# Performance work log

Measured on AMD Instinct MI355X. Metric: run time of the kernel, lower is better.

The kernel has to match this reference:

```python
import jax, jax.numpy as jnp
from jax import lax
import numpy as np

B, P, D = 32, 196, 2048   # batch, num_pixels (14x14), encoder_dim
A, E, H, V = 512, 512, 512, 10000  # attention_dim, embed_dim, decoder_dim, vocab
L = 21                    # max caption length -> T = 20 decode steps


def setup_inputs() -> dict:
    key = jax.random.key(0)
    ks = jax.random.split(key, 16)
    def n(k, shape, s=0.02):
        return jax.random.normal(k, shape, jnp.float32) * s
    def u(k, shape):
        return jax.random.uniform(k, shape, jnp.float32, -0.1, 0.1)
    caption_lengths = jnp.concatenate(
        [jnp.array([[L]], dtype=jnp.int32),
         jax.random.randint(ks[1], (B - 1, 1), 8, L + 1)], axis=0)
    return dict(
        encoder_out=jax.random.normal(ks[0], (B, P, D), jnp.float32) * 0.5,
        encoded_captions=jax.random.randint(ks[2], (B, L), 0, V),
        caption_lengths=caption_lengths,
        enc_att_w=n(ks[3], (D, A)), enc_att_b=jnp.zeros((A,), jnp.float32),
        dec_att_w=n(ks[4], (H, A)), dec_att_b=jnp.zeros((A,), jnp.float32),
        full_att_w=n(ks[5], (A,)), full_att_b=jnp.zeros((), jnp.float32),
        emb=u(ks[6], (V, E)),
        init_h_w=n(ks[7], (D, H)), init_h_b=jnp.zeros((H,), jnp.float32),
        init_c_w=n(ks[8], (D, H)), init_c_b=jnp.zeros((H,), jnp.float32),
        f_beta_w=n(ks[9], (H, D)), f_beta_b=jnp.zeros((D,), jnp.float32),
        lstm_w_ih=n(ks[10], (E + D, 4 * H)),
        lstm_w_hh=n(ks[11], (H, 4 * H)),
        lstm_b=jnp.zeros((4 * H,), jnp.float32),
        fc_w=u(ks[12], (H, V)), fc_b=jnp.zeros((V,), jnp.float32),
    )


def reference(encoder_out, encoded_captions, caption_lengths,
              enc_att_w, enc_att_b, dec_att_w, dec_att_b, full_att_w, full_att_b,
              emb, init_h_w, init_h_b, init_c_w, init_c_b,
              f_beta_w, f_beta_b, lstm_w_ih, lstm_w_hh, lstm_b, fc_w, fc_b):
    # sort batch by caption length, descending (matches torch .sort descending=True)
    lengths = caption_lengths[:, 0]
    sort_ind = jnp.argsort(-lengths)
    lengths = lengths[sort_ind]
    enc = encoder_out[sort_ind]                 # [B,P,D]
    caps = encoded_captions[sort_ind]           # [B,L]
    embs = emb[caps]                            # [B,L,E]

    mean_enc = enc.mean(axis=1)                 # [B,D]
    h0 = mean_enc @ init_h_w + init_h_b         # [B,H]
    c0 = mean_enc @ init_c_w + init_c_b

    # encoder branch of additive attention is constant across timesteps
    att1 = enc @ enc_att_w + enc_att_b          # [B,P,A]
    dec_lens = lengths - 1                      # [B]
    T = caps.shape[1] - 1

    def step(carry, xs):
        h, c = carry
        emb_t, t = xs                            # [B,E], scalar
        att2 = h @ dec_att_w + dec_att_b         # [B,A]
        e = jnp.einsum('bpa,a->bp', jax.nn.relu(att1 + att2[:, None, :]), full_att_w) + full_att_b
        alpha = jax.nn.softmax(e, axis=1)        # [B,P]
        awe = jnp.einsum('bpd,bp->bd', enc, alpha)
        gate = jax.nn.sigmoid(h @ f_beta_w + f_beta_b)
        awe = gate * awe                         # [B,D]
        x = jnp.concatenate([emb_t, awe], axis=-1)  # [B,E+D]
        g = x @ lstm_w_ih + h @ lstm_w_hh + lstm_b  # [B,4H] gates i,f,g,o
        i_g, f_g, g_g, o_g = jnp.split(g, 4, axis=-1)
        c_new = jax.nn.sigmoid(f_g) * c + jax.nn.sigmoid(i_g) * jnp.tanh(g_g)
        h_new = jax.nn.sigmoid(o_g) * jnp.tanh(c_new)
        preds = h_new @ fc_w + fc_b              # [B,V] (dropout = identity, eval mode)
        active = (t < dec_lens)[:, None]         # length-based batch slicing -> mask
        h = jnp.where(active, h_new, h)
        c = jnp.where(active, c_new, c)
        preds = jnp.where(active, preds, 0.0)
        alpha = jnp.where(active, alpha, 0.0)
        return (h, c), (preds, alpha)

    xs = (jnp.swapaxes(embs[:, :T], 0, 1), jnp.arange(T))
    (_, _), (preds, alphas) = lax.scan(step, (h0, c0), xs)
    predictions = jnp.swapaxes(preds, 0, 1)      # [B,T,V]
    alphas = jnp.swapaxes(alphas, 0, 1)          # [B,T,P]
    return predictions, caps, dec_lens, alphas, sort_ind
```

## Files before the change

kernel.cpp:

```cpp
#include <hip/hip_runtime.h>

#define B_ 32
#define P_ 196
#define D_ 2048
#define A_ 512
#define E_ 512
#define H_ 512
#define V_ 10000
#define L_ 21
#define T_ 20
#define PP 208

typedef unsigned short us;

struct KParams {
  const float* encoder_out; const int* captions; const int* cap_lens;
  const float* enc_att_w; const float* enc_att_b;
  const float* dec_att_w; const float* dec_att_b;
  const float* full_att_w; const float* full_att_b;
  const float* emb;
  const float* init_h_w; const float* init_h_b;
  const float* init_c_w; const float* init_c_b;
  const float* f_beta_w; const float* f_beta_b;
  const float* lstm_w_ih; const float* lstm_w_hh; const float* lstm_b;
  const float* fc_w; const float* fc_b;
  float* out_preds; float* out_caps; float* out_declens; float* out_alphas; float* out_sortind;
  int* sort_ind; int* declen; int* caps_s;
  us* h_bf16; float* c; us* mean_bf16;
  us* waw_bf16; us* wihE_bf16; us* embs_bf16;
  us* att1; us* Wt; us* Wt2; us* Wt3; us* encT; us* awe_bf16;
  float* gpre; float* s1out; float* alpha_g;
  int* sync;
};

__device__ __forceinline__ us f2bf(float x){
  unsigned u = __float_as_uint(x);
  unsigned r = ((u >> 16) & 1u) + 0x7FFFu;
  return (us)((u + r) >> 16);
}
__device__ __forceinline__ unsigned pack2(float a, float b){
  return (unsigned)f2bf(a) | ((unsigned)f2bf(b) << 16);
}
__device__ __forceinline__ float bf2f(unsigned u16){ return __uint_as_float(u16 << 16); }
__device__ __forceinline__ float sigm(float x){ return 1.f/(1.f + __expf(-x)); }
__device__ __forceinline__ float tanh_f(float x){ return 1.f - 2.f/(__expf(2.f*x) + 1.f); }

__device__ __forceinline__ unsigned ald(const unsigned* p){
  return __hip_atomic_load(p, __ATOMIC_RELAXED, __HIP_MEMORY_SCOPE_AGENT);
}
__device__ __forceinline__ void ast(unsigned* p, unsigned v){
  __hip_atomic_store(p, v, __ATOMIC_RELAXED, __HIP_MEMORY_SCOPE_AGENT);
}
__device__ __forceinline__ float aldf(const float* p){
  return __uint_as_float(ald((const unsigned*)p));
}
__device__ __forceinline__ void astf(float* p, float v){
  ast((unsigned*)p, __float_as_uint(v));
}

using bf16x8 = __attribute__((ext_vector_type(8))) short;
using f32x4  = __attribute__((ext_vector_type(4))) float;
#define MFMA(a,b,c) __builtin_amdgcn_mfma_f32_16x16x32_bf16((a),(b),(c),0,0,0)

#define HS 528
#define AS 2064


__global__ void k_meta(KParams p){
  __shared__ int len[32], sidx[32], sdecl[32];
  int tid = threadIdx.x;
  if (tid < 32) len[tid] = p.cap_lens[tid];
  __syncthreads();
  if (tid == 0){
    bool used[32];
    for (int i = 0; i < 32; i++) used[i] = false;
    for (int r = 0; r < 32; r++){
      int best = -1, bl = -2;
      for (int i = 0; i < 32; i++) if (!used[i] && len[i] > bl){ bl = len[i]; best = i; }
      used[best] = true; sidx[r] = best; sdecl[r] = bl - 1;
    }
  }
  __syncthreads();
  if (tid < 32){
    p.sort_ind[tid] = sidx[tid]; p.out_sortind[tid] = (float)sidx[tid];
    p.declen[tid]   = sdecl[tid]; p.out_declens[tid] = (float)sdecl[tid];
  }
  for (int idx = tid; idx < B_*L_; idx += 64){
    int b = idx / L_, l = idx - b*L_;
    int cv = p.captions[sidx[b]*L_ + l];
    p.caps_s[idx] = cv; p.out_caps[idx] = (float)cv;
  }
}

__device__ void tp64(const float* src, us* dst, int R, int C, int Rp, int bi){
  __shared__ float tl[64][68];
  int tilesC = (C + 63) >> 6;
  int tr = bi / tilesC, tc = bi - tr*tilesC;
  int r0 = tr << 6, c0 = tc << 6;
  int tid = threadIdx.x;
  {
    int r = tid >> 2, cs = (tid & 3) << 4;
    bool rok = (r0 + r) < R;
    #pragma unroll
    for (int i = 0; i < 4; i++){
      int c = c0 + cs + i*4;
      float4 v = make_float4(0.f, 0.f, 0.f, 0.f);
      if (rok && c < C) v = *(const float4*)(src + (size_t)(r0 + r)*C + c);
      *(float4*)&tl[r][cs + i*4] = v;
    }
  }
  __syncthreads();
  {
    int c = tid >> 2, rs = (tid & 3) << 4;
    if (c0 + c < C && r0 + rs < Rp){
      us tmp[16];
      #pragma unroll
      for (int i = 0; i < 16; i++) tmp[i] = f2bf(tl[rs + i][c]);
      *(uint4*)(dst + (size_t)(c0 + c)*Rp + r0 + rs)     = *(uint4*)&tmp[0];
      *(uint4*)(dst + (size_t)(c0 + c)*Rp + r0 + rs + 8) = *(uint4*)&tmp[8];
    }
  }
}

__global__ void k_prep(KParams p){
  int bi = blockIdx.x, tid = threadIdx.x;
  if (bi < 512){
    #pragma unroll
    for (int i = 0; i < 4; i++){
      int q = bi*1024 + i*256 + tid;
      const float4* src; uint2* dst; int qq;
      if (q < 262144){ src = (const float4*)p.enc_att_w; dst = (uint2*)p.waw_bf16;  qq = q; }
      else           { src = (const float4*)p.lstm_w_ih; dst = (uint2*)p.wihE_bf16; qq = q - 262144; }
      float4 v = src[qq];
      dst[qq] = make_uint2(pack2(v.x, v.y), pack2(v.z, v.w));
    }
  } else if (bi < 576){   tp64(p.dec_att_w, p.Wt,             512, 512,   512,  bi - 512);
  } else if (bi < 832){   tp64(p.f_beta_w,  p.Wt + 512*512,   512, 2048,  512,  bi - 576);
  } else if (bi < 1088){  tp64(p.lstm_w_hh, p.Wt + 2560*512,  512, 2048,  512,  bi - 832);
  } else if (bi < 2344){  tp64(p.fc_w,      p.Wt + 4608*512,  512, 10000, 512,  bi - 1088);
  } else if (bi < 3368){  tp64(p.lstm_w_ih + 512*2048, p.Wt2, 2048, 2048, 2048, bi - 2344);
  } else if (bi < 3624){  tp64(p.init_h_w,  p.Wt3,            2048, 512,  2048, bi - 3368);
  } else if (bi < 3880){  tp64(p.init_c_w,  p.Wt3 + 512*2048, 2048, 512,  2048, bi - 3624);
  } else if (bi < 4200){
    int q = (bi - 3880)*256 + tid;
    int row = q >> 7, qi = q & 127;
    int t = row >> 5, b = row & 31;
    int cap = p.caps_s[b*L_ + t];
    float4 v = ((const float4*)(p.emb + (size_t)cap*E_))[qi];
    ((uint2*)p.embs_bf16)[q] = make_uint2(pack2(v.x, v.y), pack2(v.z, v.w));
  } else {
    int bl = bi - 4200;
    int b = bl >> 7, ti = bl & 127;
    tp64(p.encoder_out + (size_t)p.sort_ind[b]*(P_*D_), p.encT + (size_t)b*D_*PP,
         196, 2048, PP, ti);
  }
}

__global__ void __launch_bounds__(256) k_gemm2(KParams p){
  __shared__ us a_lds[128][40];
  __shared__ us b_lds[128][40];
  int bi = blockIdx.x;
  const us* Aq = nullptr; const float* Af = nullptr; const int* sidx = nullptr;
  const us* Bq; const float* bias; float* C; int N, K, obf, mode, ti;
  if (bi < 196){
    Af = p.encoder_out; sidx = p.sort_ind; Bq = p.waw_bf16; bias = p.enc_att_b;
    C = (float*)p.att1; N = 512; K = 2048; obf = 1; mode = 1; ti = bi;
  } else {
    Aq = p.embs_bf16; Bq = p.wihE_bf16; bias = p.lstm_b;
    C = p.gpre; N = 2048; K = 512; obf = 0; mode = 0; ti = bi - 196;
  }
  int ntiles = N >> 7;
  int bm = (ti / ntiles) << 7;
  int bn = (ti % ntiles) << 7;
  int tid = threadIdx.x;
  int wave = tid >> 6, lane = tid & 63;
  int wr = (wave >> 1) << 6, wc = (wave & 1) << 6;
  int la = lane & 15, lq = lane >> 4;
  f32x4 acc[4][4] = {};
  for (int k0 = 0; k0 < K; k0 += 32){
    {
      int r = tid >> 1, ch = (tid & 1) << 4;
      if (mode == 0){
        const uint4* asrc = (const uint4*)(Aq + (size_t)(bm + r)*K + k0 + ch);
        uint4 v0 = asrc[0], v1 = asrc[1];
        *(uint4*)&a_lds[r][ch]     = v0;
        *(uint4*)&a_lds[r][ch + 8] = v1;
      } else {
        int g = bm + r; int b = g / 196; int pp = g - b*196;
        const float4* as = (const float4*)(Af + ((size_t)sidx[b]*196 + pp)*2048 + k0 + ch);
        float4 f0 = as[0], f1 = as[1], f2 = as[2], f3 = as[3];
        *(uint4*)&a_lds[r][ch]     = make_uint4(pack2(f0.x,f0.y), pack2(f0.z,f0.w), pack2(f1.x,f1.y), pack2(f1.z,f1.w));
        *(uint4*)&a_lds[r][ch + 8] = make_uint4(pack2(f2.x,f2.y), pack2(f2.z,f2.w), pack2(f3.x,f3.y), pack2(f3.z,f3.w));
      }
      int kk = tid >> 3, n0 = (tid & 7) << 4;
      const us* bs = Bq + (size_t)(k0 + kk)*N + bn + n0;
      uint4 bv0 = *(const uint4*)bs, bv1 = *(const uint4*)(bs + 8);
      unsigned vals[8] = {bv0.x, bv0.y, bv0.z, bv0.w, bv1.x, bv1.y, bv1.z, bv1.w};
      #pragma unroll
      for (int i = 0; i < 8; i++){
        b_lds[n0 + 2*i][kk]     = (us)(vals[i] & 0xffffu);
        b_lds[n0 + 2*i + 1][kk] = (us)(vals[i] >> 16);
      }
    }
    __syncthreads();
    bf16x8 af[4], bfr[4];
    #pragma unroll
    for (int mt = 0; mt < 4; mt++) af[mt]  = *(const bf16x8*)&a_lds[wr + mt*16 + la][lq*8];
    #pragma unroll
    for (int nt = 0; nt < 4; nt++) bfr[nt] = *(const bf16x8*)&b_lds[wc + nt*16 + la][lq*8];
    #pragma unroll
    for (int mt = 0; mt < 4; mt++)
      #pragma unroll
      for (int nt = 0; nt < 4; nt++)
        acc[mt][nt] = MFMA(af[mt], bfr[nt], acc[mt][nt]);
    __syncthreads();
  }
  #pragma unroll
  for (int mt = 0; mt < 4; mt++){
    int row0 = bm + wr + mt*16 + lq*4;
    #pragma unroll
    for (int nt = 0; nt < 4; nt++){
      int coln = bn + wc + nt*16 + la;
      float bb = bias ? bias[coln] : 0.f;
      #pragma unroll
      for (int r = 0; r < 4; r++){
        float v = acc[mt][nt][r] + bb;
        if (obf) ((us*)C)[(size_t)(row0 + r)*N + coln] = f2bf(v);
        else     C[(size_t)(row0 + r)*N + coln] = v;
      }
    }
  }
}


__device__ __forceinline__ void gsync_g(int* sc, int gen, int jb){
  __syncthreads();
  if (threadIdx.x == 0){
    int old = __hip_atomic_fetch_add(&sc[(jb & 7)*32], 1, __ATOMIC_RELEASE, __HIP_MEMORY_SCOPE_AGENT);
    bool last = false;
    if (old == gen*4 - 1){
      int old2 = __hip_atomic_fetch_add(&sc[512], 1, __ATOMIC_RELAXED, __HIP_MEMORY_SCOPE_AGENT);
      if (old2 == gen*8 - 1){
        __hip_atomic_store(&sc[544], gen, __ATOMIC_RELEASE, __HIP_MEMORY_SCOPE_AGENT);
        last = true;
      }
    }
    if (!last){
      while (__hip_atomic_load(&sc[544], __ATOMIC_RELAXED, __HIP_MEMORY_SCOPE_AGENT) < gen)
        __builtin_amdgcn_s_sleep(2);
    }
  }
  __syncthreads();
}

__device__ __forceinline__ void fc_run(const KParams& p, const int* sm_dl, const us* hlds,
                                       int b0, int slot, int nslots, int niter,
                                       int la, int lq, int tpred){
  bf16x8 afr[16];
  #pragma unroll
  for (int ks = 0; ks < 16; ks++) afr[ks] = *(const bf16x8*)&hlds[(la & 3)*HS + lq*8 + ks*32];
  for (int it = 0; it < niter; it++){
    int tile = slot + it*nslots;
    if (tile < 625){
      int n0 = tile*16;
      const us* wp = p.Wt + ((size_t)(4608 + n0 + la))*512 + lq*8;
      f32x4 ac = {};
      #pragma unroll
      for (int ks = 0; ks < 16; ks++){
        bf16x8 bB = *(const bf16x8*)(wp + ks*32);
        ac = MFMA(afr[ks], bB, ac);
      }
      if (lq == 0){
        int v = n0 + la;
        float bb = p.fc_b[v];
        #pragma unroll
        for (int r = 0; r < 4; r++){
          bool act = tpred < sm_dl[b0 + r];
          p.out_preds[((size_t)(b0 + r)*T_ + tpred)*V_ + v] = act ? (ac[r] + bb) : 0.f;
        }
      }
    }
  }
}

__global__ void __launch_bounds__(512, 2) k_loop(KParams p){
  const int tid = threadIdx.x, blk = blockIdx.x;
  const int gb = blk >> 5, jb = blk & 31, b0 = gb*4;
  const int wv = tid >> 6, lane = tid & 63, la = lane & 15, lq = lane >> 4;
  int* sc = p.sync + gb*1024;
  __shared__ float sm_att2[512], sm_fw[512], sm_red[16];
  __shared__ float sm_a4f[4*PP];
  __shared__ float gq2[4][2][16][4];
  __shared__ int sm_dl[32];
  __shared__ us sm_h[4*HS];
  __shared__ us sm_awe[4*AS];
  int gen = 0;

  if (tid < 32) sm_dl[tid] = p.declen[tid];
  __syncthreads();

  {
    int part = tid & 1, pair = tid >> 1;
    int d = jb*64 + (pair >> 2), b = b0 + (pair & 3);
    const uint4* rp = (const uint4*)(p.encT + ((size_t)b*D_ + d)*PP);
    int cs = part*13;
    float s = 0.f;
    for (int i = cs; i < cs + 13; i++){
      uint4 u = rp[i];
      s += bf2f(u.x&0xffffu)+bf2f(u.x>>16)+bf2f(u.y&0xffffu)+bf2f(u.y>>16)
         + bf2f(u.z&0xffffu)+bf2f(u.z>>16)+bf2f(u.w&0xffffu)+bf2f(u.w>>16);
    }
    s += __shfl_xor(s, 1);
    float mv = s*(1.f/196.f);
    float ov = __shfl_xor(mv, 8);
    if (part == 0 && !(tid & 8))
      ast((unsigned*)p.mean_bf16 + ((size_t)b*1024 + (d >> 1)), pack2(mv, ov));
  }
  gsync_g(sc, ++gen, jb);
  if (jb < 8){
    {
      unsigned* dst = (unsigned*)sm_awe;
      const unsigned* src = (const unsigned*)p.mean_bf16 + (size_t)b0*1024;
      for (int i = tid; i < 4096; i += 512) dst[(i >> 10)*(AS >> 1) + (i & 1023)] = ald(src + i);
    }
    __syncthreads();
    int slot = jb*8 + wv;
    const us* wp = p.Wt3 + ((size_t)(slot*16 + la))*2048 + lq*8;
    const us* ap = sm_awe + (la & 3)*AS + lq*8;
    f32x4 ac0 = {}, ac1 = {};
    for (int ki = 0; ki < 64; ki += 2){
      bf16x8 aA = *(const bf16x8*)(ap + ki*32);
      bf16x8 bB = *(const bf16x8*)(wp + ki*32);
      ac0 = MFMA(aA, bB, ac0);
      bf16x8 aA2 = *(const bf16x8*)(ap + ki*32 + 32);
      bf16x8 bB2 = *(const bf16x8*)(wp + ki*32 + 32);
      ac1 = MFMA(aA2, bB2, ac1);
    }
    f32x4 ac = ac0 + ac1;
    int col = slot*16 + la;
    if (col < 512){
      #pragma unroll
      for (int r = 0; r < 4; r++){
        float v0 = ac[r] + p.init_h_b[col];
        float v1 = __shfl_xor(v0, 1);
        if (lq == 0 && !(la & 1))
          ast((unsigned*)p.h_bf16 + (((size_t)(b0+r)*512 + col) >> 1), pack2(v0, v1));
      }
    } else {
      #pragma unroll
      for (int r = 0; r < 4; r++)
        if (lq == 0) astf(&p.c[(size_t)(b0+r)*512 + col - 512], ac[r] + p.init_c_b[col - 512]);
    }
  }
  gsync_g(sc, ++gen, jb);

  for (int t = 0; t < T_; ++t){
    {
      unsigned* dst = (unsigned*)sm_h;
      const unsigned* src = (const unsigned*)p.h_bf16 + (size_t)b0*256;
      for (int i = tid; i < 1024; i += 512) dst[(i >> 8)*(HS >> 1) + (i & 255)] = ald(src + i);
    }
    __syncthreads();
    {
      int slot = jb*8 + wv;
      bf16x8 afr[16];
      #pragma unroll
      for (int ks = 0; ks < 16; ks++) afr[ks] = *(const bf16x8*)&sm_h[(la & 3)*HS + lq*8 + ks*32];
      int tiles2[2];
      tiles2[0] = slot;
      tiles2[1] = (slot < 32) ? (256 + slot) : -1;
      #pragma unroll
      for (int it = 0; it < 2; it++){
        int tile = tiles2[it];
        if (tile >= 0){
          int n0 = tile*16;
          const us* wp = p.Wt + ((size_t)(n0 + la))*512 + lq*8;
          f32x4 ac = {};
          #pragma unroll
          for (int ks = 0; ks < 16; ks++){
            bf16x8 bB = *(const bf16x8*)(wp + ks*32);
            ac = MFMA(afr[ks], bB, ac);
          }
          if (lq == 0){
            #pragma unroll
            for (int r = 0; r < 4; r++) astf(&p.s1out[(size_t)(b0+r)*4608 + n0 + la], ac[r]);
          }
        }
      }
    }
    gsync_g(sc, ++gen, jb);
    if (jb < 4){
      int b = b0 + jb;
      for (int cc = tid; cc < 512; cc += 512){
        sm_att2[cc] = aldf(&p.s1out[(size_t)b*4608 + cc]) + p.dec_att_b[cc];
        sm_fw[cc]   = p.full_att_w[cc];
      }
      __syncthreads();
      float ee = -1e30f;
      if (tid < 196){
        const uint4* row = (const uint4*)(p.att1 + ((size_t)(b*196 + tid))*512);
        float s = 0.f;
        #pragma unroll 8
        for (int i = 0; i < 64; i++){
          uint4 u = row[i];
          float4 a0 = *(const float4*)&sm_att2[i*8], a1 = *(const float4*)&sm_att2[i*8+4];
          float4 f0 = *(const float4*)&sm_fw[i*8],   f1 = *(const float4*)&sm_fw[i*8+4];
          s += fmaxf(bf2f(u.x&0xffffu)+a0.x,0.f)*f0.x + fmaxf(bf2f(u.x>>16)+a0.y,0.f)*f0.y
             + fmaxf(bf2f(u.y&0xffffu)+a0.z,0.f)*f0.z + fmaxf(bf2f(u.y>>16)+a0.w,0.f)*f0.w
             + fmaxf(bf2f(u.z&0xffffu)+a1.x,0.f)*f1.x + fmaxf(bf2f(u.z>>16)+a1.y,0.f)*f1.y
             + fmaxf(bf2f(u.w&0xffffu)+a1.z,0.f)*f1.z + fmaxf(bf2f(u.w>>16)+a1.w,0.f)*f1.w;
        }
        ee = s;
      }
      float v = ee;
      #pragma unroll
      for (int off = 32; off; off >>= 1) v = fmaxf(v, __shfl_xor(v, off));
      if (lane == 0) sm_red[wv] = v;
      __syncthreads();
      float m = sm_red[0];
      #pragma unroll
      for (int i = 1; i < 8; i++) m = fmaxf(m, sm_red[i]);
      float ex = (tid < 196) ? __expf(ee - m) : 0.f;
      float sv = ex;
      #pragma unroll
      for (int off = 32; off; off >>= 1) sv += __shfl_xor(sv, off);
      if (lane == 0) sm_red[8 + wv] = sv;
      __syncthreads();
      float ssum = sm_red[8];
      #pragma unroll
      for (int i = 1; i < 8; i++) ssum += sm_red[8 + i];
      if (tid < 196){
        float a = ex/ssum;
        astf(&p.alpha_g[b*PP + tid], a);
        bool act = t < sm_dl[b];
        p.out_alphas[((size_t)b*T_ + t)*P_ + tid] = act ? a : 0.f;
      } else if (tid < PP) astf(&p.alpha_g[b*PP + tid], 0.f);
    } else if (t > 0){
      fc_run(p, sm_dl, sm_h, b0, (jb - 4)*8 + wv, 224, 3, la, lq, t - 1);
    }
    gsync_g(sc, ++gen, jb);
    {
      for (int i = tid; i < 4*PP; i += 512) sm_a4f[i] = aldf(&p.alpha_g[b0*PP + i]);
      __syncthreads();
      int part = tid & 1, pair = tid >> 1;
      int d = jb*64 + (pair >> 2), b = b0 + (pair & 3);
      const float* al = sm_a4f + (pair & 3)*PP;
      const uint4* rp = (const uint4*)(p.encT + ((size_t)b*D_ + d)*PP);
      int cs = part*13;
      float acc = 0.f;
      for (int i = cs; i < cs + 13; i++){
        uint4 u = rp[i];
        float4 a0 = *(const float4*)(al + i*8), a1 = *(const float4*)(al + i*8 + 4);
        acc += a0.x*bf2f(u.x&0xffffu) + a0.y*bf2f(u.x>>16)
             + a0.z*bf2f(u.y&0xffffu) + a0.w*bf2f(u.y>>16)
             + a1.x*bf2f(u.z&0xffffu) + a1.y*bf2f(u.z>>16)
             + a1.z*bf2f(u.w&0xffffu) + a1.w*bf2f(u.w>>16);
      }
      acc += __shfl_xor(acc, 1);
      float gate = sigm(aldf(&p.s1out[(size_t)b*4608 + 512 + d]) + p.f_beta_b[d]);
      float wv_ = acc*gate;
      float ov = __shfl_xor(wv_, 8);
      if (part == 0 && !(tid & 8))
        ast((unsigned*)p.awe_bf16 + ((size_t)b*1024 + (d >> 1)), pack2(wv_, ov));
    }
    gsync_g(sc, ++gen, jb);
    {
      {
        unsigned* dst = (unsigned*)sm_awe;
        const unsigned* src = (const unsigned*)p.awe_bf16 + (size_t)b0*1024;
        for (int i = tid; i < 4096; i += 512) dst[(i >> 10)*(AS >> 1) + (i & 1023)] = ald(src + i);
      }
      __syncthreads();
      int q = wv >> 1, kh = wv & 1, hc0 = jb*16;
      const us* wp = p.Wt2 + ((size_t)(q*512 + hc0 + la))*2048 + kh*1024 + lq*8;
      const us* ap = sm_awe + (la & 3)*AS + kh*1024 + lq*8;
      f32x4 ac0 = {}, ac1 = {};
      for (int ki = 0; ki < 32; ki += 2){
        bf16x8 aA = *(const bf16x8*)(ap + ki*32);
        bf16x8 bB = *(const bf16x8*)(wp + ki*32);
        ac0 = MFMA(aA, bB, ac0);
        bf16x8 aA2 = *(const bf16x8*)(ap + ki*32 + 32);
        bf16x8 bB2 = *(const bf16x8*)(wp + ki*32 + 32);
        ac1 = MFMA(aA2, bB2, ac1);
      }
      f32x4 ac = ac0 + ac1;
      if (lq == 0){
        #pragma unroll
        for (int r = 0; r < 4; r++) gq2[q][kh][la][r] = ac[r];
      }
      __syncthreads();
      if (tid < 64){
        int hc = hc0 + (tid & 15), r = tid >> 4;
        int b = b0 + r;
        float gv[4];
        #pragma unroll
        for (int qq = 0; qq < 4; qq++)
          gv[qq] = gq2[qq][0][tid & 15][r] + gq2[qq][1][tid & 15][r]
                 + aldf(&p.s1out[(size_t)b*4608 + 2560 + qq*512 + hc])
                 + p.gpre[((size_t)t*32 + b)*2048 + qq*512 + hc];
        float cold = aldf(&p.c[(size_t)b*512 + hc]);
        float cn = sigm(gv[1])*cold + sigm(gv[0])*tanh_f(gv[2]);
        float hn = sigm(gv[3])*tanh_f(cn);
        float hv1 = __shfl_xor(hn, 1);
        if (t < sm_dl[b]){
          astf(&p.c[(size_t)b*512 + hc], cn);
          if (!(tid & 1))
            ast((unsigned*)p.h_bf16 + (((size_t)b*512 + hc) >> 1), pack2(hn, hv1));
        }
      }
    }
    gsync_g(sc, ++gen, jb);
  }
  {
    unsigned* dst = (unsigned*)sm_h;
    const unsigned* src = (const unsigned*)p.h_bf16 + (size_t)b0*256;
    for (int i = tid; i < 1024; i += 512) dst[(i >> 8)*(HS >> 1) + (i & 255)] = ald(src + i);
  }
  __syncthreads();
  fc_run(p, sm_dl, sm_h, b0, jb*8 + wv, 256, 3, la, lq, T_ - 1);
}


extern "C" void kernel_launch(void* const* d_in, const int* in_sizes, int n_in,
                              void* d_out, int out_size, void* d_ws, size_t ws_size,
                              hipStream_t stream){
  (void)in_sizes; (void)n_in; (void)out_size; (void)ws_size;
  KParams p;
  p.encoder_out = (const float*)d_in[0];
  p.captions    = (const int*)d_in[1];
  p.cap_lens    = (const int*)d_in[2];
  p.enc_att_w   = (const float*)d_in[3];  p.enc_att_b = (const float*)d_in[4];
  p.dec_att_w   = (const float*)d_in[5];  p.dec_att_b = (const float*)d_in[6];
  p.full_att_w  = (const float*)d_in[7];  p.full_att_b = (const float*)d_in[8];
  p.emb         = (const float*)d_in[9];
  p.init_h_w    = (const float*)d_in[10]; p.init_h_b = (const float*)d_in[11];
  p.init_c_w    = (const float*)d_in[12]; p.init_c_b = (const float*)d_in[13];
  p.f_beta_w    = (const float*)d_in[14]; p.f_beta_b = (const float*)d_in[15];
  p.lstm_w_ih   = (const float*)d_in[16]; p.lstm_w_hh = (const float*)d_in[17]; p.lstm_b = (const float*)d_in[18];
  p.fc_w        = (const float*)d_in[19]; p.fc_b = (const float*)d_in[20];

  float* out = (float*)d_out;
  p.out_preds   = out;
  p.out_caps    = out + 6400000;
  p.out_declens = out + 6400672;
  p.out_alphas  = out + 6400704;
  p.out_sortind = out + 6526144;

  char* w = (char*)d_ws; size_t off = 0;
  auto alloc = [&](size_t bytes)->char*{ char* r = w + off; off = (off + bytes + 255) & ~(size_t)255; return r; };
  p.sort_ind  = (int*)alloc(128);
  p.declen    = (int*)alloc(128);
  p.caps_s    = (int*)alloc(2688);
  p.h_bf16    = (us*)alloc(32768);
  p.c         = (float*)alloc(65536);
  p.mean_bf16 = (us*)alloc(131072);
  p.waw_bf16  = (us*)alloc(2097152);
  p.wihE_bf16 = (us*)alloc(2097152);
  p.embs_bf16 = (us*)alloc(655360);
  p.att1      = (us*)alloc(6422528);
  p.Wt        = (us*)alloc(14958592);
  p.Wt2       = (us*)alloc(8388608);
  p.Wt3       = (us*)alloc(4194304);
  p.encT      = (us*)alloc(27262976);
  p.gpre      = (float*)alloc(5242880);
  p.s1out     = (float*)alloc(589824);
  p.alpha_g   = (float*)alloc(26624);
  p.awe_bf16  = (us*)alloc(131072);
  p.sync      = (int*)alloc(32768);

  hipMemsetAsync(p.sync, 0, 32768, stream);
  hipLaunchKernelGGL(k_meta,  dim3(1),    dim3(64),  0, stream, p);
  hipLaunchKernelGGL(k_prep,  dim3(8296), dim3(256), 0, stream, p);
  hipLaunchKernelGGL(k_gemm2, dim3(276),  dim3(256), 0, stream, p);
  void* args[] = { (void*)&p };
  hipLaunchCooperativeKernel((void*)k_loop, dim3(256), dim3(512), args, 0, stream);
}
```

Baseline: 1.571 ms.

## Fuse h-projection stage into attention/FC stage and simplify grid barrier

Removes one grid-wide barrier per decode step. The attention blocks now compute their own dec_att projection of h redundantly into shared memory. The remaining blocks compute the f_beta and w_hh projections of h together with the previous step's FC output tiles in one distributed loop. The hierarchical atomic barrier is also replaced by a single-counter spin barrier with no sleep. This cuts sync latency, but costs redundant MFMA work in the four attention blocks and more contention on the single atomic counter.

Measured after the change: 1.660 ms. 5.7% more time.

```diff
diff --git a/kernel.cpp b/kernel.cpp
--- a/kernel.cpp
+++ b/kernel.cpp
@@ -233,22 +233,11 @@
 }
 
 
-__device__ __forceinline__ void gsync_g(int* sc, int gen, int jb){
+__device__ __forceinline__ void gsync_g(int* sc, int gen){
   __syncthreads();
   if (threadIdx.x == 0){
-    int old = __hip_atomic_fetch_add(&sc[(jb & 7)*32], 1, __ATOMIC_RELEASE, __HIP_MEMORY_SCOPE_AGENT);
-    bool last = false;
-    if (old == gen*4 - 1){
-      int old2 = __hip_atomic_fetch_add(&sc[512], 1, __ATOMIC_RELAXED, __HIP_MEMORY_SCOPE_AGENT);
-      if (old2 == gen*8 - 1){
-        __hip_atomic_store(&sc[544], gen, __ATOMIC_RELEASE, __HIP_MEMORY_SCOPE_AGENT);
-        last = true;
-      }
-    }
-    if (!last){
-      while (__hip_atomic_load(&sc[544], __ATOMIC_RELAXED, __HIP_MEMORY_SCOPE_AGENT) < gen)
-        __builtin_amdgcn_s_sleep(2);
-    }
+    __hip_atomic_fetch_add(&sc[0], 1, __ATOMIC_RELEASE, __HIP_MEMORY_SCOPE_AGENT);
+    while (__hip_atomic_load(&sc[0], __ATOMIC_RELAXED, __HIP_MEMORY_SCOPE_AGENT) < gen*32) {}
   }
   __syncthreads();
 }
@@ -316,7 +305,7 @@
     if (part == 0 && !(tid & 8))
       ast((unsigned*)p.mean_bf16 + ((size_t)b*1024 + (d >> 1)), pack2(mv, ov));
   }
-  gsync_g(sc, ++gen, jb);
+  gsync_g(sc, ++gen);
   if (jb < 8){
     {
       unsigned* dst = (unsigned*)sm_awe;
@@ -352,7 +341,7 @@
         if (lq == 0) astf(&p.c[(size_t)(b0+r)*512 + col - 512], ac[r] + p.init_c_b[col - 512]);
     }
   }
-  gsync_g(sc, ++gen, jb);
+  gsync_g(sc, ++gen);
 
   for (int t = 0; t < T_; ++t){
     {
@@ -361,39 +350,23 @@
       for (int i = tid; i < 1024; i += 512) dst[(i >> 8)*(HS >> 1) + (i & 255)] = ald(src + i);
     }
     __syncthreads();
-    {
-      int slot = jb*8 + wv;
-      bf16x8 afr[16];
-      #pragma unroll
-      for (int ks = 0; ks < 16; ks++) afr[ks] = *(const bf16x8*)&sm_h[(la & 3)*HS + lq*8 + ks*32];
-      int tiles2[2];
-      tiles2[0] = slot;
-      tiles2[1] = (slot < 32) ? (256 + slot) : -1;
-      #pragma unroll
-      for (int it = 0; it < 2; it++){
-        int tile = tiles2[it];
-        if (tile >= 0){
-          int n0 = tile*16;
-          const us* wp = p.Wt + ((size_t)(n0 + la))*512 + lq*8;
-          f32x4 ac = {};
-          #pragma unroll
-          for (int ks = 0; ks < 16; ks++){
-            bf16x8 bB = *(const bf16x8*)(wp + ks*32);
-            ac = MFMA(afr[ks], bB, ac);
-          }
-          if (lq == 0){
-            #pragma unroll
-            for (int r = 0; r < 4; r++) astf(&p.s1out[(size_t)(b0+r)*4608 + n0 + la], ac[r]);
-          }
-        }
-      }
-    }
-    gsync_g(sc, ++gen, jb);
+    bf16x8 afr[16];
+    #pragma unroll
+    for (int ks = 0; ks < 16; ks++) afr[ks] = *(const bf16x8*)&sm_h[(la & 3)*HS + lq*8 + ks*32];
     if (jb < 4){
       int b = b0 + jb;
-      for (int cc = tid; cc < 512; cc += 512){
-        sm_att2[cc] = aldf(&p.s1out[(size_t)b*4608 + cc]) + p.dec_att_b[cc];
-        sm_fw[cc]   = p.full_att_w[cc];
+      for (int cc = tid; cc < 512; cc += 512) sm_fw[cc] = p.full_att_w[cc];
+      #pragma unroll
+      for (int tt = 0; tt < 4; tt++){
+        int n0 = (wv*4 + tt)*16;
+        const us* wp = p.Wt + ((size_t)(n0 + la))*512 + lq*8;
+        f32x4 ac = {};
+        #pragma unroll
+        for (int ks = 0; ks < 16; ks++){
+          bf16x8 bB = *(const bf16x8*)(wp + ks*32);
+          ac = MFMA(afr[ks], bB, ac);
+        }
+        if (lq == 0) sm_att2[n0 + la] = ac[jb] + p.dec_att_b[n0 + la];
       }
       __syncthreads();
       float ee = -1e30f;
@@ -435,10 +408,41 @@
         bool act = t < sm_dl[b];
         p.out_alphas[((size_t)b*T_ + t)*P_ + tid] = act ? a : 0.f;
       } else if (tid < PP) astf(&p.alpha_g[b*PP + tid], 0.f);
-    } else if (t > 0){
-      fc_run(p, sm_dl, sm_h, b0, (jb - 4)*8 + wv, 224, 3, la, lq, t - 1);
-    }
-    gsync_g(sc, ++gen, jb);
+    } else {
+      int slot = (jb - 4)*8 + wv;
+      #pragma unroll
+      for (int it = 0; it < 4; it++){
+        int j = slot + it*224;
+        if (j < 881){
+          bool isfc = (j >= 256);
+          if (!isfc || t > 0){
+            int row0 = isfc ? (4608 + (j - 256)*16) : ((32 + j)*16);
+            const us* wp = p.Wt + ((size_t)(row0 + la))*512 + lq*8;
+            f32x4 ac = {};
+            #pragma unroll
+            for (int ks = 0; ks < 16; ks++){
+              bf16x8 bB = *(const bf16x8*)(wp + ks*32);
+              ac = MFMA(afr[ks], bB, ac);
+            }
+            if (lq == 0){
+              if (!isfc){
+                #pragma unroll
+                for (int r = 0; r < 4; r++) astf(&p.s1out[(size_t)(b0+r)*4608 + row0 + la], ac[r]);
+              } else {
+                int vv = row0 - 4608 + la;
+                float bb = p.fc_b[vv];
+                #pragma unroll
+                for (int r = 0; r < 4; r++){
+                  bool act = (t - 1) < sm_dl[b0 + r];
+                  p.out_preds[((size_t)(b0 + r)*T_ + (t - 1))*V_ + vv] = act ? (ac[r] + bb) : 0.f;
+                }
+              }
+            }
+          }
+        }
+      }
+    }
+    gsync_g(sc, ++gen);
     {
       for (int i = tid; i < 4*PP; i += 512) sm_a4f[i] = aldf(&p.alpha_g[b0*PP + i]);
       __syncthreads();
@@ -463,7 +467,7 @@
       if (part == 0 && !(tid & 8))
         ast((unsigned*)p.awe_bf16 + ((size_t)b*1024 + (d >> 1)), pack2(wv_, ov));
     }
-    gsync_g(sc, ++gen, jb);
+    gsync_g(sc, ++gen);
     {
       {
         unsigned* dst = (unsigned*)sm_awe;
@@ -509,7 +513,7 @@
         }
       }
     }
-    gsync_g(sc, ++gen, jb);
+    gsync_g(sc, ++gen);
   }
   {
     unsigned* dst = (unsigned*)sm_h;
```

## Group eight batch rows per block group with 64 blocks per group

Applied to the files above, without the earlier changes.

Reorganizes the persistent decode kernel so each group of blocks handles 8 batch rows instead of 4, with 64 blocks per group instead of 32. MFMA tiles now use 8 of their 16 M rows, which halves how many times each weight tile is streamed per step. Every block's work partition is remapped to match: mean, attention, awe and the LSTM gate reduction. The grid barrier counts and the FC tile striding change accordingly. The risk is that the group barriers now span more blocks, and only half the blocks take part in the LSTM stage.

After: 1.559 ms. About the same (-0.7%).

```diff
diff --git a/kernel.cpp b/kernel.cpp
--- a/kernel.cpp
+++ b/kernel.cpp
@@ -238,7 +238,7 @@
   if (threadIdx.x == 0){
     int old = __hip_atomic_fetch_add(&sc[(jb & 7)*32], 1, __ATOMIC_RELEASE, __HIP_MEMORY_SCOPE_AGENT);
     bool last = false;
-    if (old == gen*4 - 1){
+    if (old == gen*8 - 1){
       int old2 = __hip_atomic_fetch_add(&sc[512], 1, __ATOMIC_RELAXED, __HIP_MEMORY_SCOPE_AGENT);
       if (old2 == gen*8 - 1){
         __hip_atomic_store(&sc[544], gen, __ATOMIC_RELEASE, __HIP_MEMORY_SCOPE_AGENT);
@@ -258,7 +258,7 @@
                                        int la, int lq, int tpred){
   bf16x8 afr[16];
   #pragma unroll
-  for (int ks = 0; ks < 16; ks++) afr[ks] = *(const bf16x8*)&hlds[(la & 3)*HS + lq*8 + ks*32];
+  for (int ks = 0; ks < 16; ks++) afr[ks] = *(const bf16x8*)&hlds[(la & 7)*HS + lq*8 + ks*32];
   for (int it = 0; it < niter; it++){
     int tile = slot + it*nslots;
     if (tile < 625){
@@ -270,13 +270,14 @@
         bf16x8 bB = *(const bf16x8*)(wp + ks*32);
         ac = MFMA(afr[ks], bB, ac);
       }
-      if (lq == 0){
+      if (lq < 2){
         int v = n0 + la;
         float bb = p.fc_b[v];
         #pragma unroll
         for (int r = 0; r < 4; r++){
-          bool act = tpred < sm_dl[b0 + r];
-          p.out_preds[((size_t)(b0 + r)*T_ + tpred)*V_ + v] = act ? (ac[r] + bb) : 0.f;
+          int b = b0 + lq*4 + r;
+          bool act = tpred < sm_dl[b];
+          p.out_preds[((size_t)b*T_ + tpred)*V_ + v] = act ? (ac[r] + bb) : 0.f;
         }
       }
     }
@@ -285,15 +286,15 @@
 
 __global__ void __launch_bounds__(512, 2) k_loop(KParams p){
   const int tid = threadIdx.x, blk = blockIdx.x;
-  const int gb = blk >> 5, jb = blk & 31, b0 = gb*4;
+  const int gb = blk >> 6, jb = blk & 63, b0 = gb*8;
   const int wv = tid >> 6, lane = tid & 63, la = lane & 15, lq = lane >> 4;
   int* sc = p.sync + gb*1024;
   __shared__ float sm_att2[512], sm_fw[512], sm_red[16];
-  __shared__ float sm_a4f[4*PP];
-  __shared__ float gq2[4][2][16][4];
+  __shared__ float sm_a4f[8*PP];
+  __shared__ float gq2[4][2][16][8];
   __shared__ int sm_dl[32];
-  __shared__ us sm_h[4*HS];
-  __shared__ us sm_awe[4*AS];
+  __shared__ us sm_h[8*HS];
+  __shared__ us sm_awe[8*AS];
   int gen = 0;
 
   if (tid < 32) sm_dl[tid] = p.declen[tid];
@@ -301,7 +302,7 @@
 
   {
     int part = tid & 1, pair = tid >> 1;
-    int d = jb*64 + (pair >> 2), b = b0 + (pair & 3);
+    int d = jb*32 + (pair >> 3), b = b0 + (pair & 7);
     const uint4* rp = (const uint4*)(p.encT + ((size_t)b*D_ + d)*PP);
     int cs = part*13;
     float s = 0.f;
@@ -312,8 +313,8 @@
     }
     s += __shfl_xor(s, 1);
     float mv = s*(1.f/196.f);
-    float ov = __shfl_xor(mv, 8);
-    if (part == 0 && !(tid & 8))
+    float ov = __shfl_xor(mv, 16);
+    if (part == 0 && !(tid & 16))
       ast((unsigned*)p.mean_bf16 + ((size_t)b*1024 + (d >> 1)), pack2(mv, ov));
   }
   gsync_g(sc, ++gen, jb);
@@ -321,12 +322,12 @@
     {
       unsigned* dst = (unsigned*)sm_awe;
       const unsigned* src = (const unsigned*)p.mean_bf16 + (size_t)b0*1024;
-      for (int i = tid; i < 4096; i += 512) dst[(i >> 10)*(AS >> 1) + (i & 1023)] = ald(src + i);
+      for (int i = tid; i < 8192; i += 512) dst[(i >> 10)*(AS >> 1) + (i & 1023)] = ald(src + i);
     }
     __syncthreads();
     int slot = jb*8 + wv;
     const us* wp = p.Wt3 + ((size_t)(slot*16 + la))*2048 + lq*8;
-    const us* ap = sm_awe + (la & 3)*AS + lq*8;
+    const us* ap = sm_awe + (la & 7)*AS + lq*8;
     f32x4 ac0 = {}, ac1 = {};
     for (int ki = 0; ki < 64; ki += 2){
       bf16x8 aA = *(const bf16x8*)(ap + ki*32);
@@ -343,13 +344,13 @@
       for (int r = 0; r < 4; r++){
         float v0 = ac[r] + p.init_h_b[col];
         float v1 = __shfl_xor(v0, 1);
-        if (lq == 0 && !(la & 1))
-          ast((unsigned*)p.h_bf16 + (((size_t)(b0+r)*512 + col) >> 1), pack2(v0, v1));
+        if (lq < 2 && !(la & 1))
+          ast((unsigned*)p.h_bf16 + (((size_t)(b0 + lq*4 + r)*512 + col) >> 1), pack2(v0, v1));
       }
     } else {
       #pragma unroll
       for (int r = 0; r < 4; r++)
-        if (lq == 0) astf(&p.c[(size_t)(b0+r)*512 + col - 512], ac[r] + p.init_c_b[col - 512]);
+        if (lq < 2) astf(&p.c[(size_t)(b0 + lq*4 + r)*512 + col - 512], ac[r] + p.init_c_b[col - 512]);
     }
   }
   gsync_g(sc, ++gen, jb);
@@ -358,38 +359,31 @@
     {
       unsigned* dst = (unsigned*)sm_h;
       const unsigned* src = (const unsigned*)p.h_bf16 + (size_t)b0*256;
-      for (int i = tid; i < 1024; i += 512) dst[(i >> 8)*(HS >> 1) + (i & 255)] = ald(src + i);
+      for (int i = tid; i < 2048; i += 512) dst[(i >> 8)*(HS >> 1) + (i & 255)] = ald(src + i);
     }
     __syncthreads();
     {
       int slot = jb*8 + wv;
-      bf16x8 afr[16];
-      #pragma unroll
-      for (int ks = 0; ks < 16; ks++) afr[ks] = *(const bf16x8*)&sm_h[(la & 3)*HS + lq*8 + ks*32];
-      int tiles2[2];
-      tiles2[0] = slot;
-      tiles2[1] = (slot < 32) ? (256 + slot) : -1;
-      #pragma unroll
-      for (int it = 0; it < 2; it++){
-        int tile = tiles2[it];
-        if (tile >= 0){
-          int n0 = tile*16;
-          const us* wp = p.Wt + ((size_t)(n0 + la))*512 + lq*8;
-          f32x4 ac = {};
+      if (slot < 288){
+        bf16x8 afr[16];
+        #pragma unroll
+        for (int ks = 0; ks < 16; ks++) afr[ks] = *(const bf16x8*)&sm_h[(la & 7)*HS + lq*8 + ks*32];
+        int n0 = slot*16;
+        const us* wp = p.Wt + ((size_t)(n0 + la))*512 + lq*8;
+        f32x4 ac = {};
+        #pragma unroll
+        for (int ks = 0; ks < 16; ks++){
+          bf16x8 bB = *(const bf16x8*)(wp + ks*32);
+          ac = MFMA(afr[ks], bB, ac);
+        }
+        if (lq < 2){
           #pragma unroll
-          for (int ks = 0; ks < 16; ks++){
-            bf16x8 bB = *(const bf16x8*)(wp + ks*32);
-            ac = MFMA(afr[ks], bB, ac);
-          }
-          if (lq == 0){
-            #pragma unroll
-            for (int r = 0; r < 4; r++) astf(&p.s1out[(size_t)(b0+r)*4608 + n0 + la], ac[r]);
-          }
+          for (int r = 0; r < 4; r++) astf(&p.s1out[(size_t)(b0 + lq*4 + r)*4608 + n0 + la], ac[r]);
         }
       }
     }
     gsync_g(sc, ++gen, jb);
-    if (jb < 4){
+    if (jb < 8){
       int b = b0 + jb;
       for (int cc = tid; cc < 512; cc += 512){
         sm_att2[cc] = aldf(&p.s1out[(size_t)b*4608 + cc]) + p.dec_att_b[cc];
@@ -436,15 +430,15 @@
         p.out_alphas[((size_t)b*T_ + t)*P_ + tid] = act ? a : 0.f;
       } else if (tid < PP) astf(&p.alpha_g[b*PP + tid], 0.f);
     } else if (t > 0){
-      fc_run(p, sm_dl, sm_h, b0, (jb - 4)*8 + wv, 224, 3, la, lq, t - 1);
+      fc_run(p, sm_dl, sm_h, b0, (jb - 8)*8 + wv, 448, 2, la, lq, t - 1);
     }
     gsync_g(sc, ++gen, jb);
     {
-      for (int i = tid; i < 4*PP; i += 512) sm_a4f[i] = aldf(&p.alpha_g[b0*PP + i]);
+      for (int i = tid; i < 8*PP; i += 512) sm_a4f[i] = aldf(&p.alpha_g[b0*PP + i]);
       __syncthreads();
       int part = tid & 1, pair = tid >> 1;
-      int d = jb*64 + (pair >> 2), b = b0 + (pair & 3);
-      const float* al = sm_a4f + (pair & 3)*PP;
+      int d = jb*32 + (pair >> 3), b = b0 + (pair & 7);
+      const float* al = sm_a4f + (pair & 7)*PP;
       const uint4* rp = (const uint4*)(p.encT + ((size_t)b*D_ + d)*PP);
       int cs = part*13;
       float acc = 0.f;
@@ -459,21 +453,21 @@
       acc += __shfl_xor(acc, 1);
       float gate = sigm(aldf(&p.s1out[(size_t)b*4608 + 512 + d]) + p.f_beta_b[d]);
       float wv_ = acc*gate;
-      float ov = __shfl_xor(wv_, 8);
-      if (part == 0 && !(tid & 8))
+      float ov = __shfl_xor(wv_, 16);
+      if (part == 0 && !(tid & 16))
         ast((unsigned*)p.awe_bf16 + ((size_t)b*1024 + (d >> 1)), pack2(wv_, ov));
     }
     gsync_g(sc, ++gen, jb);
-    {
+    if (jb < 32){
       {
         unsigned* dst = (unsigned*)sm_awe;
         const unsigned* src = (const unsigned*)p.awe_bf16 + (size_t)b0*1024;
-        for (int i = tid; i < 4096; i += 512) dst[(i >> 10)*(AS >> 1) + (i & 1023)] = ald(src + i);
+        for (int i = tid; i < 8192; i += 512) dst[(i >> 10)*(AS >> 1) + (i & 1023)] = ald(src + i);
       }
       __syncthreads();
       int q = wv >> 1, kh = wv & 1, hc0 = jb*16;
       const us* wp = p.Wt2 + ((size_t)(q*512 + hc0 + la))*2048 + kh*1024 + lq*8;
-      const us* ap = sm_awe + (la & 3)*AS + kh*1024 + lq*8;
+      const us* ap = sm_awe + (la & 7)*AS + kh*1024 + lq*8;
       f32x4 ac0 = {}, ac1 = {};
       for (int ki = 0; ki < 32; ki += 2){
         bf16x8 aA = *(const bf16x8*)(ap + ki*32);
@@ -484,12 +478,12 @@
         ac1 = MFMA(aA2, bB2, ac1);
       }
       f32x4 ac = ac0 + ac1;
-      if (lq == 0){
+      if (lq < 2){
         #pragma unroll
-        for (int r = 0; r < 4; r++) gq2[q][kh][la][r] = ac[r];
+        for (int r = 0; r < 4; r++) gq2[q][kh][la][lq*4 + r] = ac[r];
       }
       __syncthreads();
-      if (tid < 64){
+      if (tid < 128){
         int hc = hc0 + (tid & 15), r = tid >> 4;
         int b = b0 + r;
         float gv[4];
@@ -514,10 +508,10 @@
   {
     unsigned* dst = (unsigned*)sm_h;
     const unsigned* src = (const unsigned*)p.h_bf16 + (size_t)b0*256;
-    for (int i = tid; i < 1024; i += 512) dst[(i >> 8)*(HS >> 1) + (i & 255)] = ald(src + i);
-  }
-  __syncthreads();
-  fc_run(p, sm_dl, sm_h, b0, jb*8 + wv, 256, 3, la, lq, T_ - 1);
+    for (int i = tid; i < 2048; i += 512) dst[(i >> 8)*(HS >> 1) + (i & 255)] = ald(src + i);
+  }
+  __syncthreads();
+  fc_run(p, sm_dl, sm_h, b0, jb*8 + wv, 512, 2, la, lq, T_ - 1);
 }
 
 
```
